# Kernel optimization log

Measured on AMD Instinct MI355X. Metric: run time of the kernel, lower is better.

## Reference

```python
import jax, jax.numpy as jnp
import numpy as np

H, C = 5, 128          # heads, hidden_channels
NUM_GRAPHS = 500
N_NODES, N_EDGES = 20000, 320000


def gat_layer(x, edge_attr, src, dst, W, We, a_src, a_dst, a_edge, b):
    """PyG GATConv with edge_dim, add_self_loops=True, fill_value='mean', concat heads."""
    N = x.shape[0]
    ed = edge_attr.dtype
    # self-loop edge_attr = scatter-mean of incoming edge_attr per target node
    deg = jax.ops.segment_sum(jnp.ones((dst.shape[0],), ed), dst, num_segments=N)
    loop_attr = jax.ops.segment_sum(edge_attr, dst, num_segments=N) / jnp.maximum(deg, 1.0)[:, None]
    loop = jnp.arange(N, dtype=src.dtype)
    s = jnp.concatenate([src, loop])
    d = jnp.concatenate([dst, loop])
    ea = jnp.concatenate([edge_attr, loop_attr], axis=0)
    h = (x @ W).reshape(N, H, C)            # [N,H,C]
    e = (ea @ We).reshape(-1, H, C)         # [E2,H,C]
    a_l = (h * a_src).sum(-1)               # [N,H]
    a_r = (h * a_dst).sum(-1)               # [N,H]
    a_e = (e * a_edge).sum(-1)              # [E2,H]
    alpha = jax.nn.leaky_relu(a_l[s] + a_r[d] + a_e, 0.2)
    # segment softmax over destination neighborhoods
    amax = jax.ops.segment_max(alpha, d, num_segments=N)
    ex = jnp.exp(alpha - amax[d])
    denom = jax.ops.segment_sum(ex, d, num_segments=N)
    att = ex / (denom[d] + 1e-16)           # [E2,H]
    msg = h[s] * att[..., None]             # [E2,H,C]
    out = jax.ops.segment_sum(msg, d, num_segments=N).reshape(N, H * C)
    return out + b


def setup_inputs() -> dict:
    key = jax.random.key(0)
    ks = jax.random.split(key, 24)
    p = lambda k, sh: (jax.random.normal(k, sh, dtype=jnp.float32) * 0.05)
    inp = {
        "x": jax.random.normal(ks[0], (N_NODES, 43), dtype=jnp.float32),
        "edge_attr": jax.random.normal(ks[1], (N_EDGES, 10), dtype=jnp.float32),
        "W1": p(ks[2], (43, H * C)),   "We1": p(ks[3], (10, H * C)),
        "asrc1": p(ks[4], (H, C)), "adst1": p(ks[5], (H, C)), "aedge1": p(ks[6], (H, C)),
        "b1": jnp.zeros((H * C,), jnp.float32),
        "W2": p(ks[7], (H * C, H * C)), "We2": p(ks[8], (10, H * C)),
        "asrc2": p(ks[9], (H, C)), "adst2": p(ks[10], (H, C)), "aedge2": p(ks[11], (H, C)),
        "b2": jnp.zeros((H * C,), jnp.float32),
        "W3": p(ks[12], (H * C, H * C)), "We3": p(ks[13], (10, H * C)),
        "asrc3": p(ks[14], (H, C)), "adst3": p(ks[15], (H, C)), "aedge3": p(ks[16], (H, C)),
        "b3": jnp.zeros((H * C,), jnp.float32),
        "Wlin": p(ks[17], (H * C, 1)), "blin": jnp.zeros((1,), jnp.float32),
        "edge_index": jax.random.randint(ks[18], (2, N_EDGES), 0, N_NODES, dtype=jnp.int32),
        "batch": jnp.sort(jax.random.randint(ks[19], (N_NODES,), 0, NUM_GRAPHS, dtype=jnp.int32)),
    }
    return inp


def reference(x, edge_attr, W1, We1, asrc1, adst1, aedge1, b1,
              W2, We2, asrc2, adst2, aedge2, b2,
              W3, We3, asrc3, adst3, aedge3, b3,
              Wlin, blin, edge_index, batch):
    src, dst = edge_index[0], edge_index[1]
    h = jax.nn.relu(gat_layer(x, edge_attr, src, dst, W1, We1, asrc1, adst1, aedge1, b1))
    h = jax.nn.relu(gat_layer(h, edge_attr, src, dst, W2, We2, asrc2, adst2, aedge2, b2))
    h = gat_layer(h, edge_attr, src, dst, W3, We3, asrc3, adst3, aedge3, b3)
    # global mean pool over graphs
    cnt = jax.ops.segment_sum(jnp.ones((h.shape[0],), h.dtype), batch, num_segments=NUM_GRAPHS)
    pooled = jax.ops.segment_sum(h, batch, num_segments=NUM_GRAPHS) / jnp.maximum(cnt, 1.0)[:, None]
    return (pooled @ Wlin + blin).squeeze(-1)   # [NUM_GRAPHS]
```

## Files before the change

kernel.cpp:

```cpp
#include <hip/hip_runtime.h>

#define N_NODESC 20000
#define N_EDGESC 320000
#define HC 640
#define NGRAPH 500

typedef unsigned short u16;
typedef unsigned int u32;
typedef __attribute__((ext_vector_type(8))) short bf16x8;
typedef __attribute__((ext_vector_type(4))) float f32x4;

__device__ __forceinline__ float wred_sum(float v){
  #pragma unroll
  for(int o=32;o;o>>=1) v += __shfl_xor(v,o,64);
  return v;
}
__device__ __forceinline__ float lrelu(float x){ return x>0.f? x:0.2f*x; }

__device__ __forceinline__ u16 f2bf(float f){
  u32 u=__float_as_uint(f);
  u32 r=u+0x7FFFu+((u>>16)&1u);
  return (u16)(r>>16);
}
__device__ __forceinline__ float bf2f(u16 s){ return __uint_as_float(((u32)s)<<16); }
__device__ __forceinline__ float bflo(u32 w){ return __uint_as_float(w<<16); }
__device__ __forceinline__ float bfhi(u32 w){ return __uint_as_float(w&0xFFFF0000u); }

__device__ __forceinline__ void gload16(const void* g, void* l){
  __builtin_amdgcn_global_load_lds((const __attribute__((address_space(1))) void*)g,
                                   (__attribute__((address_space(3))) void*)l, 16, 0, 0);
}

__device__ __forceinline__ size_t fidx(int r, int k, int KB){
  return ((size_t)(r>>4)*KB + (k>>5))*512 + (((k>>3)&3)*16 + (r&15))*8 + (k&7);
}


__global__ void k_count(const int* __restrict__ dst, int* __restrict__ cnt){
  int i=blockIdx.x*blockDim.x+threadIdx.x;
  if(i>=N_EDGESC) return;
  atomicAdd(&cnt[dst[i]],1);
}

__global__ void k_scan(const int* __restrict__ cnt, int* __restrict__ rptr, int* __restrict__ pos){
  __shared__ int ps[1024];
  int t=threadIdx.x;
  const int CH=20;
  int beg=t*CH, end=min(beg+CH, N_NODESC);
  int s=0;
  for(int i=beg;i<end;i++) s+=cnt[i];
  ps[t]=s; __syncthreads();
  for(int off=1;off<1024;off<<=1){
    int v=(t>=off)? ps[t-off]:0;
    __syncthreads();
    ps[t]+=v;
    __syncthreads();
  }
  int base=ps[t]-s;
  for(int i=beg;i<end;i++){ rptr[i]=base; pos[i]=base; base+=cnt[i]; }
}

__global__ void k_scatter(const int* __restrict__ dst, int* __restrict__ pos,
                          int* __restrict__ eidx, int* __restrict__ dstC){
  int i=blockIdx.x*blockDim.x+threadIdx.x;
  if(i>=N_EDGESC) return;
  int d=dst[i];
  int j=atomicAdd(&pos[d],1);
  eidx[j]=i;
  dstC[j]=d;
}

__global__ void k_csr_edges(const int* __restrict__ eidx, const int* __restrict__ src,
                            const float* __restrict__ eattr,
                            int* __restrict__ srcE, float* __restrict__ eattrC){
  int j=blockIdx.x*blockDim.x+threadIdx.x;
  if(j>=N_EDGESC) return;
  int e=eidx[j];
  srcE[j]=src[e];
  const float* ep=&eattr[(size_t)e*10];
  float* op=&eattrC[(size_t)j*10];
  #pragma unroll
  for(int k=0;k<10;k++) op[k]=ep[k];
}

__global__ __launch_bounds__(256) void k_loop_attr(const float* __restrict__ eattrC,
    const int* __restrict__ rptr, const int* __restrict__ cnt,
    float* __restrict__ lattr){
  int tid=threadIdx.x, lane=tid&63;
  int n=blockIdx.x*4+(tid>>6);
  if(n>=N_NODESC) return;
  int beg=rptr[n], deg=cnt[n];
  float s[10]={0,0,0,0,0,0,0,0,0,0};
  for(int off=lane; off<deg; off+=64){
    const float* ep=&eattrC[(size_t)(beg+off)*10];
    #pragma unroll
    for(int k=0;k<10;k++) s[k]+=ep[k];
  }
  float inv=1.f/fmaxf((float)deg,1.f);
  #pragma unroll
  for(int k=0;k<10;k++){
    float tot=wred_sum(s[k]);
    if(lane==0) lattr[(size_t)n*10+k]=tot*inv;
  }
}


__global__ void k_conv_x(const float* __restrict__ x, u16* __restrict__ hi, u16* __restrict__ lo){
  int idx=blockIdx.x*blockDim.x+threadIdx.x;
  if(idx>=N_NODESC*64) return;
  int n=idx>>6, kk=idx&63;
  float v = kk<43 ? x[n*43+kk] : 0.f;
  u16 h=f2bf(v);
  size_t off=fidx(n,kk,2);
  hi[off]=h; lo[off]=f2bf(v-bf2f(h));
}

__global__ void k_conv_w3(const float* __restrict__ W0, const float* __restrict__ W1,
                          const float* __restrict__ W2,
                          u16* __restrict__ hi, u16* __restrict__ lo){
  const int R0=HC*64, R1=R0+HC*HC;
  const int TOT=R1+HC*HC;
  int idx=blockIdx.x*blockDim.x+threadIdx.x;
  if(idx>=TOT) return;
  const float* W; int local, KP, KL, base;
  if(idx<R0){ W=W0; local=idx; KP=64; KL=43; base=0; }
  else if(idx<R1){ W=W1; local=idx-R0; KP=HC; KL=HC; base=R0; }
  else { W=W2; local=idx-R1; KP=HC; KL=HC; base=R1; }
  int n=local/KP, kk=local-n*KP;
  float v = kk<KL ? W[(size_t)kk*HC+n] : 0.f;
  u16 h=f2bf(v);
  size_t off=(size_t)base + fidx(n,kk,KP>>5);
  hi[off]=h;
  lo[off]=f2bf(v-bf2f(h));
}


__global__ void k_ve3(const float* __restrict__ We0, const float* __restrict__ ae0,
                      const float* __restrict__ We1, const float* __restrict__ ae1,
                      const float* __restrict__ We2, const float* __restrict__ ae2,
                      float* __restrict__ ve3){
  int t=threadIdx.x;
  if(t>=150) return;
  int L=t/50, r=t-50*L, k=r/5, h=r%5;
  const float* We = (L==0)?We0:(L==1)?We1:We2;
  const float* ae = (L==0)?ae0:(L==1)?ae1:ae2;
  float s=0.f;
  for(int c=0;c<128;c++) s += We[k*HC + h*128 + c]*ae[h*128+c];
  ve3[t]=s;
}

__global__ void k_cb(const float* __restrict__ bias, const float* __restrict__ wlin,
                     float* __restrict__ cb){
  int lane=threadIdx.x;
  float s=0.f;
  for(int c=lane;c<HC;c+=64) s+=bias[c]*wlin[c];
  s=wred_sum(s);
  if(lane==0) cb[0]=s;
}

__global__ __launch_bounds__(256) void k_edge_terms3(const float* __restrict__ eattrC,
    const float* __restrict__ lattr, const float* __restrict__ ve3,
    float* __restrict__ aeC3, float* __restrict__ ael3){
  __shared__ float ves[150];
  if(threadIdx.x<150) ves[threadIdx.x]=ve3[threadIdx.x];
  __syncthreads();
  const int NEDGET=N_EDGESC+N_NODESC*5;
  int idx=blockIdx.x*blockDim.x+threadIdx.x;
  if(idx>=3*NEDGET) return;
  int L=idx/NEDGET, r=idx-L*NEDGET;
  const float* vl=&ves[L*50];
  if(r<N_EDGESC){
    float ev[10];
    const float* ep=&eattrC[(size_t)r*10];
    #pragma unroll
    for(int k=0;k<10;k++) ev[k]=ep[k];
    #pragma unroll
    for(int hh=0;hh<5;hh++){
      float s=0.f;
      #pragma unroll
      for(int k=0;k<10;k++) s+=ev[k]*vl[k*5+hh];
      aeC3[(size_t)L*N_EDGESC*5 + (size_t)r*5+hh]=s;
    }
  }else{
    int t=r-N_EDGESC;
    int n=t/5, h=t-5*n;
    float s=0.f;
    #pragma unroll
    for(int k=0;k<10;k++) s+=lattr[(size_t)n*10+k]*vl[k*5+h];
    ael3[(size_t)L*N_NODESC*5 + t]=s;
  }
}

__global__ void k_edgew(const int* __restrict__ srcE, const int* __restrict__ dstC,
                        const float* __restrict__ al, const float* __restrict__ ar,
                        const float* __restrict__ aeC, float* __restrict__ wE){
  int j=blockIdx.x*blockDim.x+threadIdx.x;
  if(j>=N_EDGESC) return;
  int s=srcE[j], d=dstC[j];
  const float* av=&aeC[(size_t)j*5];
  float* wp=&wE[(size_t)j*5];
  #pragma unroll
  for(int h=0;h<5;h++)
    wp[h]=__expf(lrelu(al[s*5+h]+ar[d*5+h]+av[h]));
}


__global__ __launch_bounds__(256,3) void k_gemm_l0(
    const u16* __restrict__ Ahi, const u16* __restrict__ Alo,
    const u16* __restrict__ Bhi, const u16* __restrict__ Blo,
    const float* __restrict__ asrc, const float* __restrict__ adst,
    u16* __restrict__ hb, float* __restrict__ al, float* __restrict__ ar,
    int M, int KP, int nblk){
  constexpr int TERMS=4;
  constexpr int BOFF =8192;
  __shared__ u16 lds[2*TERMS*4096];
  int tid=threadIdx.x;
  int lane=tid&63;
  int w=tid>>6;
  int l15=lane&15, lg=lane>>4;
  int orig=blockIdx.x;
  int q=nblk>>3, r=nblk&7;
  int xcd=orig&7, off=orig>>3;
  int wg=(xcd<r? xcd*(q+1) : r*(q+1)+(xcd-r)*q)+off;
  int by=wg/5, bx=wg-5*by;
  int row0=by*128, col0=bx*128;
  int wr=w>>1, wc=w&1;

  f32x4 zero = {0.f,0.f,0.f,0.f};
  f32x4 acc[4][4];
  #pragma unroll
  for(int i=0;i<4;i++)
    #pragma unroll
    for(int j=0;j<4;j++) acc[i][j]=zero;

  auto stage=[&](int b, int k0){
    u16* base = lds + b*TERMS*4096;
    int kb=k0>>5;
    #pragma unroll
    for(int c=0;c<2;c++){
      int sb=w+4*c;
      size_t af=((size_t)((row0>>4)+sb)*2 + kb)*512 + lane*8;
      size_t bf=((size_t)((col0>>4)+sb)*2 + kb)*512 + lane*8;
      gload16(Ahi+af, base + sb*512);
      gload16(Alo+af, base+4096 + sb*512);
      gload16(Bhi+bf, base+BOFF + sb*512);
      gload16(Blo+bf, base+BOFF+4096 + sb*512);
    }
  };

  int nt=KP/32;
  stage(0,0);
  __syncthreads();
  int cur=0;
  for(int t=0;t<nt;t++){
    if(t+1<nt) stage(cur^1,(t+1)*32);
    u16* cb = lds + cur*TERMS*4096;
    bf16x8 ah[4], bh[4], alv[4], bl[4];
    #pragma unroll
    for(int i=0;i<4;i++){
      ah[i]=*(const bf16x8*)&cb[(wr*4+i)*512 + lane*8];
      bh[i]=*(const bf16x8*)&cb[BOFF+(wc*4+i)*512 + lane*8];
      alv[i]=*(const bf16x8*)&cb[4096+(wr*4+i)*512+lane*8];
      bl[i] =*(const bf16x8*)&cb[BOFF+4096+(wc*4+i)*512+lane*8];
    }
    #pragma unroll
    for(int i=0;i<4;i++)
      #pragma unroll
      for(int j=0;j<4;j++){
        acc[i][j]=__builtin_amdgcn_mfma_f32_16x16x32_bf16(ah[i], bh[j],acc[i][j],0,0,0);
        acc[i][j]=__builtin_amdgcn_mfma_f32_16x16x32_bf16(alv[i],bh[j],acc[i][j],0,0,0);
        acc[i][j]=__builtin_amdgcn_mfma_f32_16x16x32_bf16(ah[i], bl[j],acc[i][j],0,0,0);
      }
    __syncthreads();
    cur^=1;
  }

  float asv[4], adv[4];
  #pragma unroll
  for(int j=0;j<4;j++){
    int c=col0+wc*64+j*16+l15;
    asv[j]=asrc[c]; adv[j]=adst[c];
  }
  #pragma unroll
  for(int i=0;i<4;i++){
    #pragma unroll
    for(int j=0;j<4;j++){
      #pragma unroll
      for(int rr=0;rr<4;rr++){
        int row=row0+wr*64+i*16+lg*4+rr;
        if(row<M) hb[(size_t)row*HC + (j*16+l15)*10 + bx*2+wc]=f2bf(acc[i][j][rr]);
      }
    }
  }
  float* redAl=(float*)lds;
  float* redAr=redAl+256;
  #pragma unroll
  for(int i=0;i<4;i++){
    #pragma unroll
    for(int rr=0;rr<4;rr++){
      float sa=0.f, sd=0.f;
      #pragma unroll
      for(int j=0;j<4;j++){ sa+=acc[i][j][rr]*asv[j]; sd+=acc[i][j][rr]*adv[j]; }
      #pragma unroll
      for(int o=1;o<16;o<<=1){ sa+=__shfl_xor(sa,o,64); sd+=__shfl_xor(sd,o,64); }
      if(l15==0){
        int lr=wr*64+i*16+lg*4+rr;
        redAl[lr*2+wc]=sa; redAr[lr*2+wc]=sd;
      }
    }
  }
  __syncthreads();
  if(tid<128){
    int row=row0+tid;
    if(row<M){
      al[(size_t)row*5+bx]=redAl[tid*2]+redAl[tid*2+1];
      ar[(size_t)row*5+bx]=redAr[tid*2]+redAr[tid*2+1];
    }
  }
}

template<bool HB, bool QOUT>
__global__ __launch_bounds__(256,6) void k_gemm64(
    const u16* __restrict__ A,
    const u16* __restrict__ B,
    const float* __restrict__ asrc, const float* __restrict__ adst,
    const float* __restrict__ wlin,
    u16* __restrict__ hb, float* __restrict__ al, float* __restrict__ ar,
    float* __restrict__ qn,
    int M, int KP, int nblk){
  __shared__ u16 lds[2*6144];
  int tid=threadIdx.x;
  int lane=tid&63;
  int w=tid>>6;
  int l15=lane&15, lg=lane>>4;
  int orig=blockIdx.x;
  int q=nblk>>3, r=nblk&7;
  int xcd=orig&7, off=orig>>3;
  int wg=(xcd<r? xcd*(q+1) : r*(q+1)+(xcd-r)*q)+off;
  int by=wg/5, bx=wg-5*by;
  int row0=by*64, col0=bx*128;
  int KB=KP>>5;

  f32x4 zero = {0.f,0.f,0.f,0.f};
  f32x4 acc[4][2];
  #pragma unroll
  for(int i=0;i<4;i++){ acc[i][0]=zero; acc[i][1]=zero; }

  auto stage=[&](int b, int k0){
    u16* base = lds + b*6144;
    int kb=k0>>5;
    size_t af=((size_t)((row0>>4)+w)*KB + kb)*512 + lane*8;
    gload16(A+af, base + w*512);
    #pragma unroll
    for(int c=0;c<2;c++){
      int sb=w+4*c;
      size_t bf=((size_t)((col0>>4)+sb)*KB + kb)*512 + lane*8;
      gload16(B+bf, base+2048 + sb*512);
    }
  };

  int nt=KP/32;
  stage(0,0);
  __syncthreads();
  int cur=0;
  for(int t=0;t<nt;t++){
    if(t+1<nt) stage(cur^1,(t+1)*32);
    u16* cb = lds + cur*6144;
    bf16x8 ah[4], bh[2];
    #pragma unroll
    for(int i=0;i<4;i++) ah[i]=*(const bf16x8*)&cb[i*512 + lane*8];
    #pragma unroll
    for(int j=0;j<2;j++) bh[j]=*(const bf16x8*)&cb[2048+(w*2+j)*512 + lane*8];
    #pragma unroll
    for(int i=0;i<4;i++){
      acc[i][0]=__builtin_amdgcn_mfma_f32_16x16x32_bf16(ah[i],bh[0],acc[i][0],0,0,0);
      acc[i][1]=__builtin_amdgcn_mfma_f32_16x16x32_bf16(ah[i],bh[1],acc[i][1],0,0,0);
    }
    __syncthreads();
    cur^=1;
  }

  float asv[2], adv[2], wlv[2];
  #pragma unroll
  for(int j=0;j<2;j++){
    int c=col0+w*32+j*16+l15;
    asv[j]=asrc[c]; adv[j]=adst[c];
    if(QOUT) wlv[j]=wlin[c];
  }
  if(HB){
    #pragma unroll
    for(int i=0;i<4;i++){
      #pragma unroll
      for(int j=0;j<2;j++){
        #pragma unroll
        for(int rr=0;rr<4;rr++){
          int row=row0+i*16+lg*4+rr;
          if(row<M)
            hb[(size_t)row*HC + ((w&1)*32+j*16+l15)*10 + bx*2+(w>>1)]=f2bf(acc[i][j][rr]);
        }
      }
    }
  }
  float* redAl=(float*)lds;
  float* redAr=redAl+256;
  float* redQ =redAr+256;
  #pragma unroll
  for(int i=0;i<4;i++){
    #pragma unroll
    for(int rr=0;rr<4;rr++){
      float sa=0.f, sd=0.f, sq=0.f;
      #pragma unroll
      for(int j=0;j<2;j++){
        sa+=acc[i][j][rr]*asv[j];
        sd+=acc[i][j][rr]*adv[j];
        if(QOUT) sq+=acc[i][j][rr]*wlv[j];
      }
      #pragma unroll
      for(int o=1;o<16;o<<=1){
        sa+=__shfl_xor(sa,o,64); sd+=__shfl_xor(sd,o,64);
        if(QOUT) sq+=__shfl_xor(sq,o,64);
      }
      if(l15==0){
        int lr=i*16+lg*4+rr;
        redAl[lr*4+w]=sa; redAr[lr*4+w]=sd;
        if(QOUT) redQ[lr*4+w]=sq;
      }
    }
  }
  __syncthreads();
  if(tid<64){
    int row=row0+tid;
    if(row<M){
      al[(size_t)row*5+bx]=redAl[tid*4]+redAl[tid*4+1]+redAl[tid*4+2]+redAl[tid*4+3];
      ar[(size_t)row*5+bx]=redAr[tid*4]+redAr[tid*4+1]+redAr[tid*4+2]+redAr[tid*4+3];
      if(QOUT) qn[(size_t)row*5+bx]=redQ[tid*4]+redQ[tid*4+1]+redQ[tid*4+2]+redQ[tid*4+3];
    }
  }
}

__global__ __launch_bounds__(256) void k_agg(const u16* __restrict__ hb, const int* __restrict__ srcE,
    const int* __restrict__ rptr, const int* __restrict__ cnt,
    const float* __restrict__ al, const float* __restrict__ ar, const float* __restrict__ ael,
    const float* __restrict__ wE, const float* __restrict__ bias,
    u16* __restrict__ ohi){
  int tid=threadIdx.x, lane=tid&63;
  int n=blockIdx.x*4+(tid>>6);
  if(n>=N_NODESC) return;
  float den[5], acc[10];
  #pragma unroll
  for(int h=0;h<5;h++)
    den[h]=__expf(lrelu(al[n*5+h]+ar[n*5+h]+ael[n*5+h]));
  {
    const u32* sp=(const u32*)(hb+(size_t)n*HC+lane*10);
    #pragma unroll
    for(int j2=0;j2<5;j2++){
      u32 wv=sp[j2];
      acc[2*j2]  =den[j2]*bflo(wv);
      acc[2*j2+1]=den[j2]*bfhi(wv);
    }
  }
  int beg=rptr[n], end=beg+cnt[n];
  int j=beg;
  for(; j+3<end; j+=4){
    int sj[4];
    #pragma unroll
    for(int u=0;u<4;u++) sj[u]=srcE[j+u];
    float w[4][5];
    #pragma unroll
    for(int u=0;u<4;u++){
      const float* wp=&wE[(size_t)(j+u)*5];
      #pragma unroll
      for(int h=0;h<5;h++) w[u][h]=wp[h];
    }
    u32 wv[4][5];
    #pragma unroll
    for(int u=0;u<4;u++){
      const u32* hr=(const u32*)(hb+(size_t)sj[u]*HC+lane*10);
      #pragma unroll
      for(int j2=0;j2<5;j2++) wv[u][j2]=hr[j2];
    }
    #pragma unroll
    for(int u=0;u<4;u++){
      #pragma unroll
      for(int j2=0;j2<5;j2++){
        den[j2]+=w[u][j2];
        acc[2*j2]  +=w[u][j2]*bflo(wv[u][j2]);
        acc[2*j2+1]+=w[u][j2]*bfhi(wv[u][j2]);
      }
    }
  }
  for(; j<end; j++){
    int sj=srcE[j];
    const float* wp=&wE[(size_t)j*5];
    float w[5];
    #pragma unroll
    for(int h=0;h<5;h++){ w[h]=wp[h]; den[h]+=w[h]; }
    const u32* hr=(const u32*)(hb+(size_t)sj*HC+lane*10);
    #pragma unroll
    for(int j2=0;j2<5;j2++){
      u32 wv=hr[j2];
      acc[2*j2]  +=w[j2]*bflo(wv);
      acc[2*j2+1]+=w[j2]*bfhi(wv);
    }
  }
  #pragma unroll
  for(int k=0;k<10;k++){
    int ccol=lane+64*k;
    float vv=acc[k]/(den[k>>1]+1e-16f)+bias[ccol];
    vv=fmaxf(vv,0.f);
    ohi[fidx(n,ccol,20)]=f2bf(vv);
  }
}

__global__ __launch_bounds__(256) void k_agg_last(const float* __restrict__ qn,
    const int* __restrict__ srcE, const int* __restrict__ rptr, const int* __restrict__ cnt,
    const float* __restrict__ al, const float* __restrict__ ar, const float* __restrict__ ael,
    const float* __restrict__ aeC, const float* __restrict__ cb,
    float* __restrict__ pnode){
  int tid=threadIdx.x;
  int sub=tid&15;
  int n=blockIdx.x*16+(tid>>4);
  if(n>=N_NODESC) return;
  float arn[5], den[5], qs[5];
  #pragma unroll
  for(int h=0;h<5;h++) arn[h]=ar[n*5+h];
  #pragma unroll
  for(int h=0;h<5;h++){ den[h]=0.f; qs[h]=0.f; }
  if(sub==0){
    #pragma unroll
    for(int h=0;h<5;h++){
      float pp=__expf(lrelu(al[n*5+h]+arn[h]+ael[n*5+h]));
      den[h]=pp; qs[h]=pp*qn[(size_t)n*5+h];
    }
  }
  int beg=rptr[n], deg=cnt[n];
  for(int off=sub; off<deg; off+=16){
    int j=beg+off;
    int s=srcE[j];
    const float* av=&aeC[(size_t)j*5];
    const float* qv=&qn[(size_t)s*5];
    #pragma unroll
    for(int h=0;h<5;h++){
      float pp=__expf(lrelu(al[s*5+h]+arn[h]+av[h]));
      den[h]+=pp; qs[h]+=pp*qv[h];
    }
  }
  #pragma unroll
  for(int h=0;h<5;h++){
    #pragma unroll
    for(int o=1;o<16;o<<=1){
      den[h]+=__shfl_xor(den[h],o,16);
      qs[h]+=__shfl_xor(qs[h],o,16);
    }
  }
  if(sub==0){
    float s=0.f;
    #pragma unroll
    for(int h=0;h<5;h++) s+=qs[h]/(den[h]+1e-16f);
    pnode[n]=s+cb[0];
  }
}

__global__ __launch_bounds__(256) void k_graphout(const float* __restrict__ pnode,
    const int* __restrict__ batch, const float* __restrict__ blin,
    float* __restrict__ out){
  int tid=threadIdx.x, lane=tid&63;
  int g=blockIdx.x*4+(tid>>6);
  if(g>=NGRAPH) return;
  auto lb=[&](int val){
    int lo=0, hi=N_NODESC;
    while(lo<hi){ int mid=(lo+hi)>>1; if(batch[mid]<val) lo=mid+1; else hi=mid; }
    return lo;
  };
  int s0=lb(g), s1=lb(g+1);
  float s=0.f;
  for(int i=s0+lane;i<s1;i+=64) s+=pnode[i];
  s=wred_sum(s);
  if(lane==0) out[g]=s/fmaxf((float)(s1-s0),1.f)+blin[0];
}


extern "C" void kernel_launch(void* const* d_in, const int* in_sizes, int n_in,
                              void* d_out, int out_size, void* d_ws, size_t ws_size,
                              hipStream_t stream){
  const float* x     = (const float*)d_in[0];
  const float* eattr = (const float*)d_in[1];
  const float* W[3]    ={(const float*)d_in[2],(const float*)d_in[8],(const float*)d_in[14]};
  const float* We[3]   ={(const float*)d_in[3],(const float*)d_in[9],(const float*)d_in[15]};
  const float* asrc[3] ={(const float*)d_in[4],(const float*)d_in[10],(const float*)d_in[16]};
  const float* adst[3] ={(const float*)d_in[5],(const float*)d_in[11],(const float*)d_in[17]};
  const float* aedge[3]={(const float*)d_in[6],(const float*)d_in[12],(const float*)d_in[18]};
  const float* bias[3] ={(const float*)d_in[7],(const float*)d_in[13],(const float*)d_in[19]};
  const float* Wlin  = (const float*)d_in[20];
  const float* blin  = (const float*)d_in[21];
  const int* eind    = (const int*)d_in[22];
  const int* srcp    = eind;
  const int* dstp    = eind + N_EDGESC;
  const int* batch   = (const int*)d_in[23];
  float* out = (float*)d_out;

  char* ws=(char*)d_ws;
  size_t o=0;
  auto alloc=[&](size_t bytes)->void*{ void* p=ws+o; o=(o+bytes+255)&~(size_t)255; return p; };
  u16* hb   =(u16*)alloc((size_t)N_NODESC*HC*2);
  u16* Ahi =(u16*)alloc((size_t)N_NODESC*HC*2);
  u16* Axhi=(u16*)alloc((size_t)N_NODESC*64*2);
  u16* Axlo=(u16*)alloc((size_t)N_NODESC*64*2);
  const int WB0=0, WB1=HC*64, WB2=WB1+HC*HC;
  u16* Bthi3=(u16*)alloc((size_t)(WB2+HC*HC)*2);
  u16* Btlo3=(u16*)alloc((size_t)(WB2+HC*HC)*2);
  float* al   =(float*)alloc((size_t)N_NODESC*5*4);
  float* ar   =(float*)alloc((size_t)N_NODESC*5*4);
  float* qn   =(float*)alloc((size_t)N_NODESC*5*4);
  float* ael3 =(float*)alloc((size_t)3*N_NODESC*5*4);
  float* aeC3 =(float*)alloc((size_t)3*N_EDGESC*5*4);
  float* wE   =(float*)alloc((size_t)N_EDGESC*5*4);
  float* lattr=(float*)alloc((size_t)N_NODESC*10*4);
  float* eattrC=(float*)alloc((size_t)N_EDGESC*10*4);
  float* ve3  =(float*)alloc(256*4);
  float* cbv  =(float*)alloc(64*4);
  float* pnode=(float*)alloc((size_t)N_NODESC*4);
  int* cntI   =(int*)alloc((size_t)N_NODESC*4);
  int* rptr   =(int*)alloc((size_t)N_NODESC*4);
  int* pos    =(int*)alloc((size_t)N_NODESC*4);
  int* eidx   =(int*)alloc((size_t)N_EDGESC*4);
  int* srcE   =(int*)alloc((size_t)N_EDGESC*4);
  int* dstC   =(int*)alloc((size_t)N_EDGESC*4);

  hipMemsetAsync(cntI,0,(size_t)N_NODESC*4,stream);

  k_count<<<(N_EDGESC+255)/256,256,0,stream>>>(dstp,cntI);
  k_scan<<<1,1024,0,stream>>>(cntI,rptr,pos);
  k_scatter<<<(N_EDGESC+255)/256,256,0,stream>>>(dstp,pos,eidx,dstC);
  k_csr_edges<<<(N_EDGESC+255)/256,256,0,stream>>>(eidx,srcp,eattr,srcE,eattrC);
  k_loop_attr<<<(N_NODESC+3)/4,256,0,stream>>>(eattrC,rptr,cntI,lattr);
  k_conv_x<<<(N_NODESC*64+255)/256,256,0,stream>>>(x,Axhi,Axlo);
  k_ve3<<<1,256,0,stream>>>(We[0],aedge[0],We[1],aedge[1],We[2],aedge[2],ve3);
  k_cb<<<1,64,0,stream>>>(bias[2],Wlin,cbv);
  {
    int tot=WB2+HC*HC;
    k_conv_w3<<<(tot+255)/256,256,0,stream>>>(W[0],W[1],W[2],Bthi3,Btlo3);
  }
  {
    const int NEDGET=N_EDGESC+N_NODESC*5;
    k_edge_terms3<<<(3*NEDGET+255)/256,256,0,stream>>>(eattrC,lattr,ve3,aeC3,ael3);
  }

  const int NBLK0=5*((N_NODESC+127)/128);
  const int NBLK64=5*((N_NODESC+63)/64);
  for(int L=0;L<3;L++){
    const float* aeL = aeC3 + (size_t)L*N_EDGESC*5;
    const float* aelL= ael3 + (size_t)L*N_NODESC*5;
    if(L==0){
      k_gemm_l0<<<NBLK0,256,0,stream>>>(Axhi,Axlo,Bthi3+WB0,Btlo3+WB0,
          asrc[L],adst[L],hb,al,ar,N_NODESC,64,NBLK0);
      k_edgew<<<(N_EDGESC+255)/256,256,0,stream>>>(srcE,dstC,al,ar,aeL,wE);
      k_agg<<<(N_NODESC+3)/4,256,0,stream>>>(hb,srcE,rptr,cntI,al,ar,aelL,wE,bias[L],Ahi);
    }else if(L==1){
      k_gemm64<true,false><<<NBLK64,256,0,stream>>>(Ahi,Bthi3+WB1,
          asrc[L],adst[L],Wlin,hb,al,ar,qn,N_NODESC,HC,NBLK64);
      k_edgew<<<(N_EDGESC+255)/256,256,0,stream>>>(srcE,dstC,al,ar,aeL,wE);
      k_agg<<<(N_NODESC+3)/4,256,0,stream>>>(hb,srcE,rptr,cntI,al,ar,aelL,wE,bias[L],Ahi);
    }else{
      k_gemm64<false,true><<<NBLK64,256,0,stream>>>(Ahi,Bthi3+WB2,
          asrc[L],adst[L],Wlin,hb,al,ar,qn,N_NODESC,HC,NBLK64);
      k_agg_last<<<(N_NODESC+15)/16,256,0,stream>>>(qn,srcE,rptr,cntI,al,ar,aelL,aeL,cbv,pnode);
    }
  }
  k_graphout<<<(NGRAPH+3)/4,256,0,stream>>>(pnode,batch,blin,out);
}
```

Measured before the change: 411.4 us.

## Aggregate raw layer-0 features before projection and fold attention vectors into W0

Layer 0 now aggregates the 43-wide padded input features per destination for each head, and only then multiplies by W0. Before, it projected every node to 640 channels and then gathered those 640-wide rows. The attention logits al/ar are computed directly from x using precomputed W0·a_src and W0·a_dst vectors, which removes the GEMM epilogue reductions. The softmax normalisation, bias and ReLU move into the new GEMM epilogue. The aggregated activations are stored as single-term bf16 instead of a hi/lo split, which lowers precision in exchange for fewer MFMAs and less gather traffic.

New measurement: 393.9 us. -4.3%, faster.

```diff
diff --git a/kernel.cpp b/kernel.cpp
--- a/kernel.cpp
+++ b/kernel.cpp
@@ -105,14 +105,11 @@
 }
 
 
-__global__ void k_conv_x(const float* __restrict__ x, u16* __restrict__ hi, u16* __restrict__ lo){
+__global__ void k_padx(const float* __restrict__ x, float* __restrict__ xp){
   int idx=blockIdx.x*blockDim.x+threadIdx.x;
   if(idx>=N_NODESC*64) return;
   int n=idx>>6, kk=idx&63;
-  float v = kk<43 ? x[n*43+kk] : 0.f;
-  u16 h=f2bf(v);
-  size_t off=fidx(n,kk,2);
-  hi[off]=h; lo[off]=f2bf(v-bf2f(h));
+  xp[idx] = kk<43 ? x[n*43+kk] : 0.f;
 }
 
 __global__ void k_conv_w3(const float* __restrict__ W0, const float* __restrict__ W1,
@@ -149,6 +146,42 @@
   ve3[t]=s;
 }
 
+__global__ void k_vs0(const float* __restrict__ W0, const float* __restrict__ asrc,
+                      const float* __restrict__ adst,
+                      float* __restrict__ VS, float* __restrict__ VD){
+  int t=threadIdx.x;
+  if(t>=320) return;
+  int k=t/5, h=t%5;
+  float sv=0.f, dv=0.f;
+  if(k<43){
+    for(int c=0;c<128;c++){
+      float wv=W0[(size_t)k*HC + h*128 + c];
+      sv+=wv*asrc[h*128+c];
+      dv+=wv*adst[h*128+c];
+    }
+  }
+  VS[t]=sv; VD[t]=dv;
+}
+
+__global__ __launch_bounds__(256) void k_alar0(const float* __restrict__ x,
+    const float* __restrict__ VS, const float* __restrict__ VD,
+    float* __restrict__ al, float* __restrict__ ar){
+  __shared__ float vs[320], vd[320];
+  if(threadIdx.x<320){ vs[threadIdx.x]=VS[threadIdx.x]; vd[threadIdx.x]=VD[threadIdx.x]; }
+  __syncthreads();
+  int idx=blockIdx.x*blockDim.x+threadIdx.x;
+  if(idx>=N_NODESC*5) return;
+  int n=idx/5, h=idx-5*n;
+  float sa=0.f, sd=0.f;
+  const float* xr=&x[(size_t)n*43];
+  for(int k=0;k<43;k++){
+    float xv=xr[k];
+    sa+=xv*vs[k*5+h];
+    sd+=xv*vd[k*5+h];
+  }
+  al[idx]=sa; ar[idx]=sd;
+}
+
 __global__ void k_cb(const float* __restrict__ bias, const float* __restrict__ wlin,
                      float* __restrict__ cb){
   int lane=threadIdx.x;
@@ -205,15 +238,65 @@
 }
 
 
-__global__ __launch_bounds__(256,3) void k_gemm_l0(
-    const u16* __restrict__ Ahi, const u16* __restrict__ Alo,
+__global__ __launch_bounds__(256) void k_aggx(const float* __restrict__ xp,
+    const int* __restrict__ srcE, const int* __restrict__ rptr, const int* __restrict__ cnt,
+    const float* __restrict__ al, const float* __restrict__ ar, const float* __restrict__ ael,
+    const float* __restrict__ wE,
+    u16* __restrict__ aggx, float* __restrict__ den0){
+  const size_t HSZ=(size_t)N_NODESC*64;
+  int tid=threadIdx.x, lane=tid&63;
+  int n=blockIdx.x*4+(tid>>6);
+  if(n>=N_NODESC) return;
+  float den[5], acc[5];
+  #pragma unroll
+  for(int h=0;h<5;h++)
+    den[h]=__expf(lrelu(al[n*5+h]+ar[n*5+h]+ael[n*5+h]));
+  float xn=xp[(size_t)n*64+lane];
+  #pragma unroll
+  for(int h=0;h<5;h++) acc[h]=den[h]*xn;
+  int beg=rptr[n], end=beg+cnt[n];
+  int j=beg;
+  for(; j+7<end; j+=8){
+    int sj[8]; float xv[8];
+    #pragma unroll
+    for(int u=0;u<8;u++) sj[u]=srcE[j+u];
+    #pragma unroll
+    for(int u=0;u<8;u++) xv[u]=xp[(size_t)sj[u]*64+lane];
+    #pragma unroll
+    for(int u=0;u<8;u++){
+      const float* wp=&wE[(size_t)(j+u)*5];
+      #pragma unroll
+      for(int h=0;h<5;h++){
+        float w=wp[h];
+        den[h]+=w;
+        acc[h]+=w*xv[u];
+      }
+    }
+  }
+  for(; j<end; j++){
+    int sj=srcE[j];
+    float xv=xp[(size_t)sj*64+lane];
+    const float* wp=&wE[(size_t)j*5];
+    #pragma unroll
+    for(int h=0;h<5;h++){
+      float w=wp[h];
+      den[h]+=w;
+      acc[h]+=w*xv;
+    }
+  }
+  size_t fo=fidx(n,lane,2);
+  #pragma unroll
+  for(int h=0;h<5;h++) aggx[(size_t)h*HSZ+fo]=f2bf(acc[h]);
+  if(lane<5) den0[(size_t)n*5+lane]=den[lane];
+}
+
+__global__ __launch_bounds__(256,3) void k_gemm_l0b(
+    const u16* __restrict__ AGX,
     const u16* __restrict__ Bhi, const u16* __restrict__ Blo,
-    const float* __restrict__ asrc, const float* __restrict__ adst,
-    u16* __restrict__ hb, float* __restrict__ al, float* __restrict__ ar,
-    int M, int KP, int nblk){
-  constexpr int TERMS=4;
-  constexpr int BOFF =8192;
-  __shared__ u16 lds[2*TERMS*4096];
+    const float* __restrict__ den0, const float* __restrict__ bias,
+    u16* __restrict__ A1, int M, int nblk){
+  const size_t HSZ=(size_t)N_NODESC*64;
+  __shared__ u16 lds[2*3*4096];
   int tid=threadIdx.x;
   int lane=tid&63;
   int w=tid>>6;
@@ -225,6 +308,7 @@
   int by=wg/5, bx=wg-5*by;
   int row0=by*128, col0=bx*128;
   int wr=w>>1, wc=w&1;
+  const u16* A=AGX+(size_t)bx*HSZ;
 
   f32x4 zero = {0.f,0.f,0.f,0.f};
   f32x4 acc[4][4];
@@ -234,90 +318,63 @@
     for(int j=0;j<4;j++) acc[i][j]=zero;
 
   auto stage=[&](int b, int k0){
-    u16* base = lds + b*TERMS*4096;
+    u16* base = lds + b*3*4096;
     int kb=k0>>5;
     #pragma unroll
     for(int c=0;c<2;c++){
       int sb=w+4*c;
       size_t af=((size_t)((row0>>4)+sb)*2 + kb)*512 + lane*8;
       size_t bf=((size_t)((col0>>4)+sb)*2 + kb)*512 + lane*8;
-      gload16(Ahi+af, base + sb*512);
-      gload16(Alo+af, base+4096 + sb*512);
-      gload16(Bhi+bf, base+BOFF + sb*512);
-      gload16(Blo+bf, base+BOFF+4096 + sb*512);
+      gload16(A+af, base + sb*512);
+      gload16(Bhi+bf, base+4096 + sb*512);
+      gload16(Blo+bf, base+8192 + sb*512);
     }
   };
 
-  int nt=KP/32;
   stage(0,0);
   __syncthreads();
   int cur=0;
-  for(int t=0;t<nt;t++){
-    if(t+1<nt) stage(cur^1,(t+1)*32);
-    u16* cb = lds + cur*TERMS*4096;
-    bf16x8 ah[4], bh[4], alv[4], bl[4];
+  for(int t=0;t<2;t++){
+    if(t==0) stage(1,32);
+    u16* cb = lds + cur*3*4096;
+    bf16x8 ah[4], bh[4], bl[4];
     #pragma unroll
     for(int i=0;i<4;i++){
       ah[i]=*(const bf16x8*)&cb[(wr*4+i)*512 + lane*8];
-      bh[i]=*(const bf16x8*)&cb[BOFF+(wc*4+i)*512 + lane*8];
-      alv[i]=*(const bf16x8*)&cb[4096+(wr*4+i)*512+lane*8];
-      bl[i] =*(const bf16x8*)&cb[BOFF+4096+(wc*4+i)*512+lane*8];
+      bh[i]=*(const bf16x8*)&cb[4096+(wc*4+i)*512 + lane*8];
+      bl[i]=*(const bf16x8*)&cb[8192+(wc*4+i)*512 + lane*8];
     }
     #pragma unroll
     for(int i=0;i<4;i++)
       #pragma unroll
       for(int j=0;j<4;j++){
-        acc[i][j]=__builtin_amdgcn_mfma_f32_16x16x32_bf16(ah[i], bh[j],acc[i][j],0,0,0);
-        acc[i][j]=__builtin_amdgcn_mfma_f32_16x16x32_bf16(alv[i],bh[j],acc[i][j],0,0,0);
-        acc[i][j]=__builtin_amdgcn_mfma_f32_16x16x32_bf16(ah[i], bl[j],acc[i][j],0,0,0);
+        acc[i][j]=__builtin_amdgcn_mfma_f32_16x16x32_bf16(ah[i],bh[j],acc[i][j],0,0,0);
+        acc[i][j]=__builtin_amdgcn_mfma_f32_16x16x32_bf16(ah[i],bl[j],acc[i][j],0,0,0);
       }
     __syncthreads();
     cur^=1;
   }
 
-  float asv[4], adv[4];
-  #pragma unroll
-  for(int j=0;j<4;j++){
-    int c=col0+wc*64+j*16+l15;
-    asv[j]=asrc[c]; adv[j]=adst[c];
-  }
   #pragma unroll
   for(int i=0;i<4;i++){
     #pragma unroll
     for(int j=0;j<4;j++){
+      int col=col0+wc*64+j*16+l15;
+      float bv=bias[col];
       #pragma unroll
       for(int rr=0;rr<4;rr++){
         int row=row0+wr*64+i*16+lg*4+rr;
-        if(row<M) hb[(size_t)row*HC + (j*16+l15)*10 + bx*2+wc]=f2bf(acc[i][j][rr]);
+        if(row<M){
+          float dv=den0[(size_t)row*5+bx];
+          float v=acc[i][j][rr]/(dv+1e-16f)+bv;
+          v=fmaxf(v,0.f);
+          A1[fidx(row,col,20)]=f2bf(v);
+        }
       }
     }
   }
-  float* redAl=(float*)lds;
-  float* redAr=redAl+256;
-  #pragma unroll
-  for(int i=0;i<4;i++){
-    #pragma unroll
-    for(int rr=0;rr<4;rr++){
-      float sa=0.f, sd=0.f;
-      #pragma unroll
-      for(int j=0;j<4;j++){ sa+=acc[i][j][rr]*asv[j]; sd+=acc[i][j][rr]*adv[j]; }
-      #pragma unroll
-      for(int o=1;o<16;o<<=1){ sa+=__shfl_xor(sa,o,64); sd+=__shfl_xor(sd,o,64); }
-      if(l15==0){
-        int lr=wr*64+i*16+lg*4+rr;
-        redAl[lr*2+wc]=sa; redAr[lr*2+wc]=sd;
-      }
-    }
-  }
-  __syncthreads();
-  if(tid<128){
-    int row=row0+tid;
-    if(row<M){
-      al[(size_t)row*5+bx]=redAl[tid*2]+redAl[tid*2+1];
-      ar[(size_t)row*5+bx]=redAr[tid*2]+redAr[tid*2+1];
-    }
-  }
-}
+}
+
 
 template<bool HB, bool QOUT>
 __global__ __launch_bounds__(256,6) void k_gemm64(
@@ -604,20 +661,23 @@
   auto alloc=[&](size_t bytes)->void*{ void* p=ws+o; o=(o+bytes+255)&~(size_t)255; return p; };
   u16* hb   =(u16*)alloc((size_t)N_NODESC*HC*2);
   u16* Ahi =(u16*)alloc((size_t)N_NODESC*HC*2);
-  u16* Axhi=(u16*)alloc((size_t)N_NODESC*64*2);
-  u16* Axlo=(u16*)alloc((size_t)N_NODESC*64*2);
+  float* xp =(float*)alloc((size_t)N_NODESC*64*4);
+  u16* aggx=(u16*)alloc((size_t)5*N_NODESC*64*2);
   const int WB0=0, WB1=HC*64, WB2=WB1+HC*HC;
   u16* Bthi3=(u16*)alloc((size_t)(WB2+HC*HC)*2);
   u16* Btlo3=(u16*)alloc((size_t)(WB2+HC*HC)*2);
   float* al   =(float*)alloc((size_t)N_NODESC*5*4);
   float* ar   =(float*)alloc((size_t)N_NODESC*5*4);
   float* qn   =(float*)alloc((size_t)N_NODESC*5*4);
+  float* den0 =(float*)alloc((size_t)N_NODESC*5*4);
   float* ael3 =(float*)alloc((size_t)3*N_NODESC*5*4);
   float* aeC3 =(float*)alloc((size_t)3*N_EDGESC*5*4);
   float* wE   =(float*)alloc((size_t)N_EDGESC*5*4);
   float* lattr=(float*)alloc((size_t)N_NODESC*10*4);
   float* eattrC=(float*)alloc((size_t)N_EDGESC*10*4);
   float* ve3  =(float*)alloc(256*4);
+  float* VS0  =(float*)alloc(320*4);
+  float* VD0  =(float*)alloc(320*4);
   float* cbv  =(float*)alloc(64*4);
   float* pnode=(float*)alloc((size_t)N_NODESC*4);
   int* cntI   =(int*)alloc((size_t)N_NODESC*4);
@@ -634,8 +694,9 @@
   k_scatter<<<(N_EDGESC+255)/256,256,0,stream>>>(dstp,pos,eidx,dstC);
   k_csr_edges<<<(N_EDGESC+255)/256,256,0,stream>>>(eidx,srcp,eattr,srcE,eattrC);
   k_loop_attr<<<(N_NODESC+3)/4,256,0,stream>>>(eattrC,rptr,cntI,lattr);
-  k_conv_x<<<(N_NODESC*64+255)/256,256,0,stream>>>(x,Axhi,Axlo);
+  k_padx<<<(N_NODESC*64+255)/256,256,0,stream>>>(x,xp);
   k_ve3<<<1,256,0,stream>>>(We[0],aedge[0],We[1],aedge[1],We[2],aedge[2],ve3);
+  k_vs0<<<1,320,0,stream>>>(W[0],asrc[0],adst[0],VS0,VD0);
   k_cb<<<1,64,0,stream>>>(bias[2],Wlin,cbv);
   {
     int tot=WB2+HC*HC;
@@ -645,27 +706,29 @@
     const int NEDGET=N_EDGESC+N_NODESC*5;
     k_edge_terms3<<<(3*NEDGET+255)/256,256,0,stream>>>(eattrC,lattr,ve3,aeC3,ael3);
   }
+  k_alar0<<<(N_NODESC*5+255)/256,256,0,stream>>>(x,VS0,VD0,al,ar);
 
   const int NBLK0=5*((N_NODESC+127)/128);
   const int NBLK64=5*((N_NODESC+63)/64);
-  for(int L=0;L<3;L++){
-    const float* aeL = aeC3 + (size_t)L*N_EDGESC*5;
-    const float* aelL= ael3 + (size_t)L*N_NODESC*5;
-    if(L==0){
-      k_gemm_l0<<<NBLK0,256,0,stream>>>(Axhi,Axlo,Bthi3+WB0,Btlo3+WB0,
-          asrc[L],adst[L],hb,al,ar,N_NODESC,64,NBLK0);
-      k_edgew<<<(N_EDGESC+255)/256,256,0,stream>>>(srcE,dstC,al,ar,aeL,wE);
-      k_agg<<<(N_NODESC+3)/4,256,0,stream>>>(hb,srcE,rptr,cntI,al,ar,aelL,wE,bias[L],Ahi);
-    }else if(L==1){
-      k_gemm64<true,false><<<NBLK64,256,0,stream>>>(Ahi,Bthi3+WB1,
-          asrc[L],adst[L],Wlin,hb,al,ar,qn,N_NODESC,HC,NBLK64);
-      k_edgew<<<(N_EDGESC+255)/256,256,0,stream>>>(srcE,dstC,al,ar,aeL,wE);
-      k_agg<<<(N_NODESC+3)/4,256,0,stream>>>(hb,srcE,rptr,cntI,al,ar,aelL,wE,bias[L],Ahi);
-    }else{
-      k_gemm64<false,true><<<NBLK64,256,0,stream>>>(Ahi,Bthi3+WB2,
-          asrc[L],adst[L],Wlin,hb,al,ar,qn,N_NODESC,HC,NBLK64);
-      k_agg_last<<<(N_NODESC+15)/16,256,0,stream>>>(qn,srcE,rptr,cntI,al,ar,aelL,aeL,cbv,pnode);
-    }
+
+  k_edgew<<<(N_EDGESC+255)/256,256,0,stream>>>(srcE,dstC,al,ar,aeC3,wE);
+  k_aggx<<<(N_NODESC+3)/4,256,0,stream>>>(xp,srcE,rptr,cntI,al,ar,ael3,wE,aggx,den0);
+  k_gemm_l0b<<<NBLK0,256,0,stream>>>(aggx,Bthi3+WB0,Btlo3+WB0,den0,bias[0],Ahi,N_NODESC,NBLK0);
+
+  {
+    const float* aeL = aeC3 + (size_t)1*N_EDGESC*5;
+    const float* aelL= ael3 + (size_t)1*N_NODESC*5;
+    k_gemm64<true,false><<<NBLK64,256,0,stream>>>(Ahi,Bthi3+WB1,
+        asrc[1],adst[1],Wlin,hb,al,ar,qn,N_NODESC,HC,NBLK64);
+    k_edgew<<<(N_EDGESC+255)/256,256,0,stream>>>(srcE,dstC,al,ar,aeL,wE);
+    k_agg<<<(N_NODESC+3)/4,256,0,stream>>>(hb,srcE,rptr,cntI,al,ar,aelL,wE,bias[1],Ahi);
+  }
+  {
+    const float* aeL = aeC3 + (size_t)2*N_EDGESC*5;
+    const float* aelL= ael3 + (size_t)2*N_NODESC*5;
+    k_gemm64<false,true><<<NBLK64,256,0,stream>>>(Ahi,Bthi3+WB2,
+        asrc[2],adst[2],Wlin,hb,al,ar,qn,N_NODESC,HC,NBLK64);
+    k_agg_last<<<(N_NODESC+15)/16,256,0,stream>>>(qn,srcE,rptr,cntI,al,ar,aelL,aeC3+(size_t)2*N_EDGESC*5,cbv,pnode);
   }
   k_graphout<<<(NGRAPH+3)/4,256,0,stream>>>(pnode,batch,blin,out);
 }
```
